# Kernel optimization log

Measured on AMD Instinct MI355X. Metric: run time of the kernel, lower is better.

Reference implementation:

```python
import jax, jax.numpy as jnp
import numpy as np

NUM_EMBEDDINGS = 1024
EMBEDDING_DIM = 256
E_LOSS_WEIGHT = 0.25
MU = 0.01
EPSILON = 1e-05
N_TOKENS = 65536


def setup_inputs() -> dict:
    key = jax.random.key(0)
    k1, k2, k3 = jax.random.split(key, 3)
    return {
        "inputs": jax.random.normal(k1, (N_TOKENS, EMBEDDING_DIM), dtype=jnp.float32),
        "embedding_weight": jax.random.normal(k2, (NUM_EMBEDDINGS, EMBEDDING_DIM), dtype=jnp.float32),
        "ema_w": jax.random.normal(k3, (NUM_EMBEDDINGS, EMBEDDING_DIM), dtype=jnp.float32),
        "ema_cluster_size": jnp.zeros((NUM_EMBEDDINGS,), dtype=jnp.float32),
    }


def reference(inputs, embedding_weight, ema_w, ema_cluster_size):
    N, D = inputs.shape
    K = embedding_weight.shape[0]

    # Squared L2 distances: [N, K]
    distances = (
        jnp.sum(inputs ** 2, axis=1, keepdims=True)
        + jnp.sum(embedding_weight ** 2, axis=1)
        - 2.0 * (inputs @ embedding_weight.T)
    )
    idx = jnp.argmin(distances, axis=1)              # [N]

    # Gather codebook entries (replaces one-hot @ weight)
    quantized_raw = embedding_weight[idx]            # [N, D]

    # Commitment loss (quantized detached)
    e_latent_loss = jnp.mean((jax.lax.stop_gradient(quantized_raw) - inputs) ** 2)
    loss = E_LOSS_WEIGHT * e_latent_loss

    # Per-code counts and scatter-sum of inputs (replaces one-hot matmuls)
    counts = jax.ops.segment_sum(jnp.ones((N,), inputs.dtype), idx, num_segments=K)  # [K]
    dw = jax.ops.segment_sum(inputs, idx, num_segments=K)                             # [K, D]

    # EMA updates (training branch)
    new_cluster = ema_cluster_size * (1.0 - MU) + MU * counts
    n = jnp.sum(new_cluster)
    new_cluster = (new_cluster + EPSILON) / (n + K * EPSILON) * n
    new_ema_w = ema_w * (1.0 - MU) + MU * dw
    new_embedding = new_ema_w / new_cluster[:, None]

    # Straight-through estimator
    quantized = inputs + jax.lax.stop_gradient(quantized_raw - inputs)

    avg_probs = counts / N
    perplexity = jnp.exp(-jnp.sum(avg_probs * jnp.log(avg_probs + 1e-10)))

    encoding_indices = idx.reshape(N, 1)
    return quantized, loss, encoding_indices, perplexity, new_cluster, new_ema_w, new_embedding
```

## Files before the change

kernel.cpp:

```cpp
#include <hip/hip_runtime.h>

typedef _Float16 half8 __attribute__((ext_vector_type(8)));
typedef _Float16 half4 __attribute__((ext_vector_type(4)));
typedef float f32x4 __attribute__((ext_vector_type(4)));

#define N_TOK 65536
#define DIM   256
#define KCODE 1024
#define MU_C  0.01f
#define EPS_C 1e-5f

#define O_Q    0
#define O_LOSS 16777216
#define O_IDX  16777217
#define O_PERP 16842753
#define O_NC   16842754
#define O_NEW  16843778
#define O_EMB  17105922

#define W_IDX   0
#define W_CNT   65536
#define W_CUR   66560
#define W_OFF   67584
#define W_CNTF  68608
#define W_NFLAG 69632
#define W_ELAT  69633
#define W_FLAG  69696
#define W_ORDER 135232
#define W_DW    200768
#define W_WSQ   462912
#define W_WH    463936
#define W_XSQF  595008
#define W_ELATA 660544
#define W_PACK  676928

__device__ __forceinline__ int imin(int a, int b) { return a < b ? a : b; }
__device__ __forceinline__ int imax(int a, int b) { return a > b ? a : b; }

__global__ void convert_wsq(const float* __restrict__ W, _Float16* __restrict__ Wh,
                            float* __restrict__ wsq) {
    int gid = blockIdx.x * 256 + threadIdx.x;
    int row = gid >> 6, lane = gid & 63;
    float4 v = *(const float4*)(W + (size_t)row * 256 + lane * 4);
    half4 h;
    h[0] = (_Float16)v.x; h[1] = (_Float16)v.y; h[2] = (_Float16)v.z; h[3] = (_Float16)v.w;
    *(half4*)(Wh + (size_t)row * 256 + lane * 4) = h;
    float s = v.x * v.x + v.y * v.y + v.z * v.z + v.w * v.w;
#pragma unroll
    for (int off = 1; off < 64; off <<= 1) s += __shfl_xor(s, off);
    if (lane == 0) wsq[row] = s;
}

__global__ __launch_bounds__(256, 2) void argmin_mfma(
    const float* __restrict__ X, const _Float16* __restrict__ Wh,
    const float* __restrict__ wsq, unsigned long long* __restrict__ halfres)
{
    __shared__ _Float16 Bs[2][32 * 256];

    const int tid  = threadIdx.x;
    const int lane = tid & 63;
    const int w    = tid >> 6;
    const int l15  = lane & 15;
    const int lk   = lane >> 4;
    const int half  = blockIdx.x & 1;
    const int cbase = half * 512;
    const int t0    = (blockIdx.x >> 1) * 256;

    half8 a[4][8];
#pragma unroll
    for (int g2 = 0; g2 < 4; ++g2) {
        const float* xr = X + (size_t)(t0 + w * 64 + g2 * 16 + l15) * 256 + lk * 8;
#pragma unroll
        for (int g = 0; g < 8; ++g) {
            float4 u0 = *(const float4*)(xr + g * 32);
            float4 u1 = *(const float4*)(xr + g * 32 + 4);
            half8 h;
            h[0] = (_Float16)u0.x; h[1] = (_Float16)u0.y;
            h[2] = (_Float16)u0.z; h[3] = (_Float16)u0.w;
            h[4] = (_Float16)u1.x; h[5] = (_Float16)u1.y;
            h[6] = (_Float16)u1.z; h[7] = (_Float16)u1.w;
            a[g2][g] = h;
        }
    }

    int u1a[16], u2a[16];
#pragma unroll
    for (int i = 0; i < 16; ++i) { u1a[i] = 0x7FFFFFFF; u2a[i] = 0x7FFFFFFF; }

#define STAGE(cc, bb)                                                          \
    _Pragma("unroll")                                                          \
    for (int i = 0; i < 4; ++i) {                                              \
        int loff = (w * 4 + i) * 1024;                                         \
        int off  = loff + lane * 16;                                           \
        int row  = off >> 9;                                                   \
        int slot = (off >> 4) & 31;                                            \
        const _Float16* src = Wh + (size_t)(cbase + (cc) * 32 + row) * 256     \
                                 + ((slot ^ row) << 3);                        \
        __builtin_amdgcn_global_load_lds(                                      \
            (const __attribute__((address_space(1))) void*)src,                \
            (__attribute__((address_space(3))) void*)((char*)Bs[bb] + loff),   \
            16, 0, 0);                                                         \
    }

    STAGE(0, 0);
    __syncthreads();

    for (int c = 0; c < 16; ++c) {
        const int cur = c & 1;
        if (c < 15) { STAGE(c + 1, cur ^ 1); }

        f32x4 acc[4][2];
#pragma unroll
        for (int g2 = 0; g2 < 4; ++g2) { acc[g2][0] = (f32x4)0.0f; acc[g2][1] = (f32x4)0.0f; }

        __builtin_amdgcn_s_setprio(1);
#pragma unroll
        for (int ks = 0; ks < 8; ++ks) {
            const int j = ks * 4 + lk;
            const char* base = (const char*)Bs[cur];
            half8 b0 = *(const half8*)(base + l15 * 512        + ((j ^ l15) << 4));
            half8 b1 = *(const half8*)(base + (16 + l15) * 512 + ((j ^ (16 + l15)) << 4));
#pragma unroll
            for (int g2 = 0; g2 < 4; ++g2) {
                acc[g2][0] = __builtin_amdgcn_mfma_f32_16x16x32_f16(
                    a[g2][ks], b0, acc[g2][0], 0, 0, 0);
                acc[g2][1] = __builtin_amdgcn_mfma_f32_16x16x32_f16(
                    a[g2][ks], b1, acc[g2][1], 0, 0, 0);
            }
        }
        __builtin_amdgcn_s_setprio(0);

#pragma unroll
        for (int nf = 0; nf < 2; ++nf) {
            int   code = cbase + c * 32 + nf * 16 + l15;
            float tc   = fmaf(0.5f, wsq[code], 512.0f);
#pragma unroll
            for (int g2 = 0; g2 < 4; ++g2)
#pragma unroll
                for (int r = 0; r < 4; ++r) {
                    float sv = tc - acc[g2][nf][r];
                    int u = (__float_as_int(sv) & 0xFFFFFC00) | code;
                    int s = g2 * 4 + r;
                    u2a[s] = imin(u2a[s], imax(u1a[s], u));
                    u1a[s] = imin(u1a[s], u);
                }
        }
        __syncthreads();
    }
#undef STAGE

#pragma unroll
    for (int s = 0; s < 16; ++s) {
#pragma unroll
        for (int off = 1; off < 16; off <<= 1) {
            int b1 = __shfl_xor(u1a[s], off);
            int b2 = __shfl_xor(u2a[s], off);
            int n2 = imin(imin(u2a[s], b2), imax(u1a[s], b1));
            u1a[s] = imin(u1a[s], b1);
            u2a[s] = n2;
        }
    }
    if (l15 == 0) {
#pragma unroll
        for (int s = 0; s < 16; ++s) {
            int row = t0 + w * 64 + (s >> 2) * 16 + lk * 4 + (s & 3);
            halfres[(size_t)half * 65536 + row] =
                ((unsigned long long)(unsigned)u1a[s] << 32) | (unsigned)u2a[s];
        }
    }
}

__global__ void merge_halves(const unsigned long long* __restrict__ halfres,
                             int* __restrict__ idx_out,
                             unsigned* __restrict__ nflag, int* __restrict__ flaglist)
{
    int t = blockIdx.x * 256 + threadIdx.x;
    unsigned long long A = halfres[t], B = halfres[65536 + t];
    int a1 = (int)(A >> 32), a2 = (int)(unsigned)A;
    int b1 = (int)(B >> 32), b2 = (int)(unsigned)B;
    int u1 = imin(a1, b1);
    int u2 = imin(imax(a1, b1), imin(a2, b2));
    idx_out[t] = u1 & 1023;
    float s1 = __int_as_float(u1 & 0xFFFFFC00);
    float s2 = __int_as_float(u2 & 0xFFFFFC00);
    if (s2 - s1 < 0.125f) {
        unsigned p = atomicAdd(nflag, 1u);
        flaglist[p] = t;
    }
}

__global__ void cleanup_xsq(const float* __restrict__ X,
                            const unsigned* __restrict__ nflagp,
                            const int* __restrict__ flaglist,
                            float* __restrict__ xsqf) {
    int n = (int)nflagp[0];
    int wid  = (blockIdx.x * 256 + threadIdx.x) >> 6;
    int lane = threadIdx.x & 63;
    for (int i = wid; i < n; i += 1024) {
        const float* row = X + (size_t)flaglist[i] * 256;
        float4 v = *(const float4*)(row + lane * 4);
        float s = v.x * v.x + v.y * v.y + v.z * v.z + v.w * v.w;
#pragma unroll
        for (int off = 1; off < 64; off <<= 1) s += __shfl_xor(s, off);
        if (lane == 0) xsqf[i] = s;
    }
}

__global__ __launch_bounds__(256, 2) void cleanup_gemm(
    const float* __restrict__ X, const float* __restrict__ W,
    const float* __restrict__ wsq, const unsigned* __restrict__ nflagp,
    const int* __restrict__ flaglist, const float* __restrict__ xsqf,
    unsigned long long* __restrict__ pack)
{
    __shared__ float xs [16][64];
    __shared__ float wps[16][128];
    __shared__ float wsq_s[128];

    const int n = (int)nflagp[0];
    const int tid = threadIdx.x;
    const int tx  = tid & 15;
    const int ty  = tid >> 4;
    const int c0    = (blockIdx.x & 7) * 128;
    const int tslot = blockIdx.x >> 3;
    const int srow_x = tid & 63,  sq_x = tid >> 6;
    const int srow_w = tid & 127, sh_w = tid >> 7;

    if (tid < 128) wsq_s[tid] = wsq[c0 + tid];

    for (int tile = tslot; tile * 64 < n; tile += 256) {
        const int t0 = tile * 64;
        const int gtok = flaglist[imin(t0 + srow_x, n - 1)];
        const float* xrow = X + (size_t)gtok * DIM;
        const float* wrow = W + (size_t)(c0 + srow_w) * DIM + sh_w * 8;

        float xsq_r[4];
#pragma unroll
        for (int i = 0; i < 4; ++i) xsq_r[i] = xsqf[imin(t0 + ty * 4 + i, n - 1)];

        float minv[4]; int mini[4];
#pragma unroll
        for (int i = 0; i < 4; ++i) { minv[i] = 3.402823466e+38f; mini[i] = 0; }

        float acc[4][8];
#pragma unroll
        for (int i = 0; i < 4; ++i)
#pragma unroll
            for (int j = 0; j < 8; ++j) acc[i][j] = 0.0f;

        float4 xa = *(const float4*)(xrow + sq_x * 4);
        float4 wa = *(const float4*)(wrow);
        float4 wb = *(const float4*)(wrow + 4);

        for (int ks = 0; ks < 16; ++ks) {
            __syncthreads();
            xs[sq_x * 4 + 0][srow_x] = xa.x; xs[sq_x * 4 + 1][srow_x] = xa.y;
            xs[sq_x * 4 + 2][srow_x] = xa.z; xs[sq_x * 4 + 3][srow_x] = xa.w;
            wps[sh_w * 8 + 0][srow_w] = wa.x; wps[sh_w * 8 + 1][srow_w] = wa.y;
            wps[sh_w * 8 + 2][srow_w] = wa.z; wps[sh_w * 8 + 3][srow_w] = wa.w;
            wps[sh_w * 8 + 4][srow_w] = wb.x; wps[sh_w * 8 + 5][srow_w] = wb.y;
            wps[sh_w * 8 + 6][srow_w] = wb.z; wps[sh_w * 8 + 7][srow_w] = wb.w;
            __syncthreads();
            if (ks < 15) {
                xa = *(const float4*)(xrow + (ks + 1) * 16 + sq_x * 4);
                wa = *(const float4*)(wrow + (ks + 1) * 16);
                wb = *(const float4*)(wrow + (ks + 1) * 16 + 4);
            }
#pragma unroll
            for (int kl = 0; kl < 16; ++kl) {
                float4 av = *(const float4*)&xs [kl][ty * 4];
                float4 b0 = *(const float4*)&wps[kl][tx * 8];
                float4 b1 = *(const float4*)&wps[kl][tx * 8 + 4];
                float aa[4] = {av.x, av.y, av.z, av.w};
                float bb[8] = {b0.x, b0.y, b0.z, b0.w, b1.x, b1.y, b1.z, b1.w};
#pragma unroll
                for (int i = 0; i < 4; ++i)
#pragma unroll
                    for (int j = 0; j < 8; ++j)
                        acc[i][j] = fmaf(aa[i], bb[j], acc[i][j]);
            }
        }
#pragma unroll
        for (int i = 0; i < 4; ++i) {
#pragma unroll
            for (int j = 0; j < 8; ++j) {
                float t1 = xsq_r[i] + wsq_s[tx * 8 + j];
                float s  = t1 - 2.0f * acc[i][j];
                int   cc = c0 + tx * 8 + j;
                if (s < minv[i]) { minv[i] = s; mini[i] = cc; }
            }
        }
#pragma unroll
        for (int i = 0; i < 4; ++i) {
#pragma unroll
            for (int off = 1; off < 16; off <<= 1) {
                float ov = __shfl_xor(minv[i], off);
                int   oi = __shfl_xor(mini[i], off);
                if (ov < minv[i] || (ov == minv[i] && oi < mini[i])) {
                    minv[i] = ov; mini[i] = oi;
                }
            }
        }
        if (tx == 0) {
#pragma unroll
            for (int i = 0; i < 4; ++i) {
                int pos = t0 + ty * 4 + i;
                if (pos < n) {
                    unsigned long long pu =
                        ((unsigned long long)(unsigned)__float_as_int(minv[i]) << 32)
                        | (unsigned)mini[i];
                    atomicMin(&pack[pos], pu);
                }
            }
        }
        __syncthreads();
    }
}

__global__ void cleanup_write(const unsigned* __restrict__ nflagp,
                              const int* __restrict__ flaglist,
                              const unsigned long long* __restrict__ pack,
                              int* __restrict__ idx_out) {
    int n = (int)nflagp[0];
    for (int i = blockIdx.x * 256 + threadIdx.x; i < n; i += 65536)
        idx_out[flaglist[i]] = (int)(pack[i] & 0xFFFFFFFFull);
}

__global__ __launch_bounds__(256) void epilogue_token(
    const float* __restrict__ X, const float* __restrict__ W,
    const int* __restrict__ idx, float* __restrict__ out,
    float* __restrict__ elat_arr, unsigned* __restrict__ cnt)
{
    int gid = blockIdx.x * 256 + threadIdx.x;
    int t = gid >> 6, q = gid & 63;
    int code = idx[t];
    float4 x4 = ((const float4*)X)[gid];
    float4 w4 = ((const float4*)W)[(size_t)code * 64 + q];
    ((float4*)(out + O_Q))[gid] = w4;
    float dx0 = w4.x - x4.x, dx1 = w4.y - x4.y, dx2 = w4.z - x4.z, dx3 = w4.w - x4.w;
    float e = dx0 * dx0 + dx1 * dx1 + dx2 * dx2 + dx3 * dx3;
    if (q == 0) {
        out[O_IDX + t] = (float)code;
        atomicAdd(&cnt[code], 1u);
    }
#pragma unroll
    for (int off = 1; off < 64; off <<= 1) e += __shfl_xor(e, off);
    __shared__ float se[4];
    int lane = threadIdx.x & 63, wid = threadIdx.x >> 6;
    if (lane == 0) se[wid] = e;
    __syncthreads();
    if (threadIdx.x == 0) elat_arr[blockIdx.x] = se[0] + se[1] + se[2] + se[3];
}

__global__ __launch_bounds__(256) void k_scan(const unsigned* __restrict__ cnt,
                                              unsigned* __restrict__ offs,
                                              float* __restrict__ cntf) {
    int t = threadIdx.x, lane = t & 63, wid = t >> 6;
    uint4 v = ((const uint4*)cnt)[t];
    cntf[4 * t + 0] = (float)v.x; cntf[4 * t + 1] = (float)v.y;
    cntf[4 * t + 2] = (float)v.z; cntf[4 * t + 3] = (float)v.w;
    unsigned s = v.x + v.y + v.z + v.w;
    unsigned ps = s;
#pragma unroll
    for (int off = 1; off < 64; off <<= 1) {
        unsigned o = __shfl_up(ps, off);
        if (lane >= off) ps += o;
    }
    __shared__ unsigned wsum[4];
    if (lane == 63) wsum[wid] = ps;
    __syncthreads();
    unsigned base = 0;
#pragma unroll
    for (int i = 0; i < 4; ++i) if (i < wid) base += wsum[i];
    unsigned excl = base + ps - s;
    offs[4 * t + 0] = excl;
    offs[4 * t + 1] = excl + v.x;
    offs[4 * t + 2] = excl + v.x + v.y;
    offs[4 * t + 3] = excl + v.x + v.y + v.z;
}

__global__ void k_scatter(const int* __restrict__ idx, const unsigned* __restrict__ offs,
                          unsigned* __restrict__ cursor, int* __restrict__ order) {
    int t = blockIdx.x * 256 + threadIdx.x;
    int c = idx[t];
    unsigned p = atomicAdd(&cursor[c], 1u);
    order[offs[c] + p] = t;
}

__global__ __launch_bounds__(256) void k_dw(const float* __restrict__ X,
                                            const int* __restrict__ order,
                                            const int* __restrict__ idx,
                                            float* __restrict__ dw)
{
    int gw   = (blockIdx.x * 256 + threadIdx.x) >> 6;
    int lane = threadIdx.x & 63;
    int p0 = gw * 16;
    float4 acc = make_float4(0.f, 0.f, 0.f, 0.f);
    int cur = -1;
#pragma unroll 4
    for (int i = 0; i < 16; ++i) {
        int t = order[p0 + i];
        int c = idx[t];
        float4 x4 = *(const float4*)(X + (size_t)t * 256 + lane * 4);
        if (c != cur) {
            if (cur >= 0) {
                float* dwp = dw + (size_t)cur * 256 + lane * 4;
                atomicAdd(dwp + 0, acc.x); atomicAdd(dwp + 1, acc.y);
                atomicAdd(dwp + 2, acc.z); atomicAdd(dwp + 3, acc.w);
            }
            cur = c; acc = x4;
        } else {
            acc.x += x4.x; acc.y += x4.y; acc.z += x4.z; acc.w += x4.w;
        }
    }
    if (cur >= 0) {
        float* dwp = dw + (size_t)cur * 256 + lane * 4;
        atomicAdd(dwp + 0, acc.x); atomicAdd(dwp + 1, acc.y);
        atomicAdd(dwp + 2, acc.z); atomicAdd(dwp + 3, acc.w);
    }
}

__global__ __launch_bounds__(1024) void finalize_small(
    const float* __restrict__ ecs, const float* __restrict__ counts,
    const float* __restrict__ elat_arr, float* __restrict__ out)
{
    int k = threadIdx.x;
    float cnt = counts[k];
    float nc = ecs[k] * (1.0f - MU_C) + MU_C * cnt;
    float p = cnt * (1.0f / 65536.0f);
    float h = p * logf(p + 1e-10f);
    float el = 0.f;
#pragma unroll
    for (int i = 0; i < 16; ++i) el += elat_arr[k + i * 1024];
    float rn = nc, rh = h, re = el;
#pragma unroll
    for (int off = 1; off < 64; off <<= 1) {
        rn += __shfl_xor(rn, off);
        rh += __shfl_xor(rh, off);
        re += __shfl_xor(re, off);
    }
    __shared__ float sn[16], sh[16], sef[16];
    int wid = k >> 6, lane = k & 63;
    if (lane == 0) { sn[wid] = rn; sh[wid] = rh; sef[wid] = re; }
    __syncthreads();
    float n = 0.0f, H = 0.0f, E = 0.0f;
#pragma unroll
    for (int i = 0; i < 16; ++i) { n += sn[i]; H += sh[i]; E += sef[i]; }
    out[O_NC + k] = (nc + EPS_C) / (n + 1024.0f * EPS_C) * n;
    if (k == 0) {
        out[O_LOSS] = 0.25f * (E * (1.0f / 16777216.0f));
        out[O_PERP] = expf(-H);
    }
}

__global__ void finalize_embed(const float* __restrict__ ema_w,
                               const float* __restrict__ dw, float* __restrict__ out)
{
    int gid = blockIdx.x * blockDim.x + threadIdx.x;
    int k = gid >> 8;
    float ew = ema_w[gid] * (1.0f - MU_C) + MU_C * dw[gid];
    out[O_NEW + gid] = ew;
    out[O_EMB + gid] = ew / out[O_NC + k];
}

extern "C" void kernel_launch(void* const* d_in, const int* in_sizes, int n_in,
                              void* d_out, int out_size, void* d_ws, size_t ws_size,
                              hipStream_t stream) {
    const float* X     = (const float*)d_in[0];
    const float* W     = (const float*)d_in[1];
    const float* ema_w = (const float*)d_in[2];
    const float* ecs   = (const float*)d_in[3];
    float*    out    = (float*)d_out;
    unsigned* wsu    = (unsigned*)d_ws;
    float*    wsf    = (float*)d_ws;
    int*      idx    = (int*)d_ws + W_IDX;
    unsigned* cnt    = wsu + W_CNT;
    unsigned* cursor = wsu + W_CUR;
    unsigned* offs   = wsu + W_OFF;
    float*    cntf   = wsf + W_CNTF;
    unsigned* nflag  = wsu + W_NFLAG;
    int*      flags  = (int*)d_ws + W_FLAG;
    int*      order  = (int*)d_ws + W_ORDER;
    float*    dw     = wsf + W_DW;
    float*    wsq    = wsf + W_WSQ;
    _Float16* Wh     = (_Float16*)(wsu + W_WH);
    float*    xsqf   = wsf + W_XSQF;
    float*    elatA  = wsf + W_ELATA;
    unsigned long long* pack    = (unsigned long long*)(wsu + W_PACK);
    unsigned long long* halfres = (unsigned long long*)(wsf + W_DW);

    hipMemsetAsync(wsu + W_CNT, 0, 4098 * sizeof(unsigned), stream);
    hipMemsetAsync(pack, 0xFF, 65536 * sizeof(unsigned long long), stream);
    hipLaunchKernelGGL(convert_wsq,    dim3(256),   dim3(256),  0, stream, W, Wh, wsq);
    hipLaunchKernelGGL(argmin_mfma,    dim3(512),   dim3(256),  0, stream, X, Wh, wsq, halfres);
    hipLaunchKernelGGL(merge_halves,   dim3(256),   dim3(256),  0, stream, halfres, idx, nflag, flags);
    hipMemsetAsync(wsf + W_DW, 0, 262144 * sizeof(float), stream);
    hipLaunchKernelGGL(cleanup_xsq,    dim3(256),   dim3(256),  0, stream, X, nflag, flags, xsqf);
    hipLaunchKernelGGL(cleanup_gemm,   dim3(2048),  dim3(256),  0, stream, X, W, wsq, nflag, flags, xsqf, pack);
    hipLaunchKernelGGL(cleanup_write,  dim3(256),   dim3(256),  0, stream, nflag, flags, pack, idx);
    hipLaunchKernelGGL(epilogue_token, dim3(16384), dim3(256),  0, stream, X, W, idx, out, elatA, cnt);
    hipLaunchKernelGGL(k_scan,         dim3(1),     dim3(256),  0, stream, cnt, offs, cntf);
    hipLaunchKernelGGL(k_scatter,      dim3(256),   dim3(256),  0, stream, idx, offs, cursor, order);
    hipLaunchKernelGGL(k_dw,           dim3(1024),  dim3(256),  0, stream, X, order, idx, dw);
    hipLaunchKernelGGL(finalize_small, dim3(1),     dim3(1024), 0, stream, ecs, cntf, elatA, out);
    hipLaunchKernelGGL(finalize_embed, dim3(1024),  dim3(256),  0, stream, ema_w, dw, out);
}
```

Baseline: 240.3 us.

## Fuse token epilogue into sorted dw pass and fold memsets into convert kernel

The per-token epilogue (quantized write, commitment error, histogram) is folded into the sorted dw accumulation kernel, so X is read once for both outputs. A separate histogram kernel counts codes, and the order array packs code and token to avoid an extra idx lookup. The three memsets move into convert_wsq, which removes API calls, and the argmin loop swaps __syncthreads for explicit vmcnt waits plus raw barriers. In exchange, quantized rows are written in sorted order, which scatters the stores, and halfres now needs its own workspace region.

```diff
diff --git a/kernel.cpp b/kernel.cpp
--- a/kernel.cpp
+++ b/kernel.cpp
@@ -24,7 +24,6 @@
 #define W_OFF   67584
 #define W_CNTF  68608
 #define W_NFLAG 69632
-#define W_ELAT  69633
 #define W_FLAG  69696
 #define W_ORDER 135232
 #define W_DW    200768
@@ -33,12 +32,13 @@
 #define W_XSQF  595008
 #define W_ELATA 660544
 #define W_PACK  676928
+#define W_HALF  808000
 
 __device__ __forceinline__ int imin(int a, int b) { return a < b ? a : b; }
 __device__ __forceinline__ int imax(int a, int b) { return a > b ? a : b; }
 
 __global__ void convert_wsq(const float* __restrict__ W, _Float16* __restrict__ Wh,
-                            float* __restrict__ wsq) {
+                            float* __restrict__ wsq, unsigned* __restrict__ wsu) {
     int gid = blockIdx.x * 256 + threadIdx.x;
     int row = gid >> 6, lane = gid & 63;
     float4 v = *(const float4*)(W + (size_t)row * 256 + lane * 4);
@@ -49,6 +49,9 @@
 #pragma unroll
     for (int off = 1; off < 64; off <<= 1) s += __shfl_xor(s, off);
     if (lane == 0) wsq[row] = s;
+    if (gid < 4097) wsu[W_CNT + gid] = 0u;
+    ((float4*)(wsu + W_DW))[gid] = make_float4(0.f, 0.f, 0.f, 0.f);
+    ((unsigned long long*)(wsu + W_PACK))[gid] = ~0ull;
 }
 
 __global__ __launch_bounds__(256, 2) void argmin_mfma(
@@ -103,11 +106,16 @@
     }
 
     STAGE(0, 0);
-    __syncthreads();
 
     for (int c = 0; c < 16; ++c) {
         const int cur = c & 1;
-        if (c < 15) { STAGE(c + 1, cur ^ 1); }
+        if (c < 15) {
+            STAGE(c + 1, cur ^ 1);
+            asm volatile("s_waitcnt vmcnt(4)" ::: "memory");
+        } else {
+            asm volatile("s_waitcnt vmcnt(0)" ::: "memory");
+        }
+        __builtin_amdgcn_s_barrier();
 
         f32x4 acc[4][2];
 #pragma unroll
@@ -145,7 +153,7 @@
                     u1a[s] = imin(u1a[s], u);
                 }
         }
-        __syncthreads();
+        __builtin_amdgcn_s_barrier();
     }
 #undef STAGE
 
@@ -171,7 +179,7 @@
 }
 
 __global__ void merge_halves(const unsigned long long* __restrict__ halfres,
-                             int* __restrict__ idx_out,
+                             int* __restrict__ idx_out, float* __restrict__ out,
                              unsigned* __restrict__ nflag, int* __restrict__ flaglist)
 {
     int t = blockIdx.x * 256 + threadIdx.x;
@@ -181,6 +189,7 @@
     int u1 = imin(a1, b1);
     int u2 = imin(imax(a1, b1), imin(a2, b2));
     idx_out[t] = u1 & 1023;
+    out[O_IDX + t] = (float)(u1 & 1023);
     float s1 = __int_as_float(u1 & 0xFFFFFC00);
     float s2 = __int_as_float(u2 & 0xFFFFFC00);
     if (s2 - s1 < 0.125f) {
@@ -319,36 +328,19 @@
 __global__ void cleanup_write(const unsigned* __restrict__ nflagp,
                               const int* __restrict__ flaglist,
                               const unsigned long long* __restrict__ pack,
-                              int* __restrict__ idx_out) {
+                              int* __restrict__ idx_out, float* __restrict__ out) {
     int n = (int)nflagp[0];
-    for (int i = blockIdx.x * 256 + threadIdx.x; i < n; i += 65536)
-        idx_out[flaglist[i]] = (int)(pack[i] & 0xFFFFFFFFull);
-}
-
-__global__ __launch_bounds__(256) void epilogue_token(
-    const float* __restrict__ X, const float* __restrict__ W,
-    const int* __restrict__ idx, float* __restrict__ out,
-    float* __restrict__ elat_arr, unsigned* __restrict__ cnt)
-{
-    int gid = blockIdx.x * 256 + threadIdx.x;
-    int t = gid >> 6, q = gid & 63;
-    int code = idx[t];
-    float4 x4 = ((const float4*)X)[gid];
-    float4 w4 = ((const float4*)W)[(size_t)code * 64 + q];
-    ((float4*)(out + O_Q))[gid] = w4;
-    float dx0 = w4.x - x4.x, dx1 = w4.y - x4.y, dx2 = w4.z - x4.z, dx3 = w4.w - x4.w;
-    float e = dx0 * dx0 + dx1 * dx1 + dx2 * dx2 + dx3 * dx3;
-    if (q == 0) {
+    for (int i = blockIdx.x * 256 + threadIdx.x; i < n; i += 65536) {
+        int t = flaglist[i];
+        int code = (int)(pack[i] & 0xFFFFFFFFull);
+        idx_out[t] = code;
         out[O_IDX + t] = (float)code;
-        atomicAdd(&cnt[code], 1u);
-    }
-#pragma unroll
-    for (int off = 1; off < 64; off <<= 1) e += __shfl_xor(e, off);
-    __shared__ float se[4];
-    int lane = threadIdx.x & 63, wid = threadIdx.x >> 6;
-    if (lane == 0) se[wid] = e;
-    __syncthreads();
-    if (threadIdx.x == 0) elat_arr[blockIdx.x] = se[0] + se[1] + se[2] + se[3];
+    }
+}
+
+__global__ void k_hist(const int* __restrict__ idx, unsigned* __restrict__ cnt) {
+    int t = blockIdx.x * 256 + threadIdx.x;
+    atomicAdd(&cnt[idx[t]], 1u);
 }
 
 __global__ __launch_bounds__(256) void k_scan(const unsigned* __restrict__ cnt,
@@ -379,27 +371,29 @@
 }
 
 __global__ void k_scatter(const int* __restrict__ idx, const unsigned* __restrict__ offs,
-                          unsigned* __restrict__ cursor, int* __restrict__ order) {
+                          unsigned* __restrict__ cursor, unsigned* __restrict__ order) {
     int t = blockIdx.x * 256 + threadIdx.x;
     int c = idx[t];
     unsigned p = atomicAdd(&cursor[c], 1u);
-    order[offs[c] + p] = t;
-}
-
-__global__ __launch_bounds__(256) void k_dw(const float* __restrict__ X,
-                                            const int* __restrict__ order,
-                                            const int* __restrict__ idx,
-                                            float* __restrict__ dw)
+    order[offs[c] + p] = ((unsigned)c << 16) | (unsigned)t;
+}
+
+__global__ __launch_bounds__(256) void k_epilogue_dw(
+    const float* __restrict__ X, const float* __restrict__ W,
+    const unsigned* __restrict__ order, float* __restrict__ out,
+    float* __restrict__ dw, float* __restrict__ elat_arr)
 {
     int gw   = (blockIdx.x * 256 + threadIdx.x) >> 6;
     int lane = threadIdx.x & 63;
     int p0 = gw * 16;
     float4 acc = make_float4(0.f, 0.f, 0.f, 0.f);
+    float4 wreg = make_float4(0.f, 0.f, 0.f, 0.f);
     int cur = -1;
+    float e = 0.f;
 #pragma unroll 4
     for (int i = 0; i < 16; ++i) {
-        int t = order[p0 + i];
-        int c = idx[t];
+        unsigned u = order[p0 + i];
+        int t = (int)(u & 0xFFFFu), c = (int)(u >> 16);
         float4 x4 = *(const float4*)(X + (size_t)t * 256 + lane * 4);
         if (c != cur) {
             if (cur >= 0) {
@@ -407,16 +401,28 @@
                 atomicAdd(dwp + 0, acc.x); atomicAdd(dwp + 1, acc.y);
                 atomicAdd(dwp + 2, acc.z); atomicAdd(dwp + 3, acc.w);
             }
+            wreg = *(const float4*)(W + (size_t)c * 256 + lane * 4);
             cur = c; acc = x4;
         } else {
             acc.x += x4.x; acc.y += x4.y; acc.z += x4.z; acc.w += x4.w;
         }
+        ((float4*)(out + O_Q))[(size_t)t * 64 + lane] = wreg;
+        float d0 = wreg.x - x4.x, d1 = wreg.y - x4.y;
+        float d2 = wreg.z - x4.z, d3 = wreg.w - x4.w;
+        e += d0 * d0 + d1 * d1 + d2 * d2 + d3 * d3;
     }
     if (cur >= 0) {
         float* dwp = dw + (size_t)cur * 256 + lane * 4;
         atomicAdd(dwp + 0, acc.x); atomicAdd(dwp + 1, acc.y);
         atomicAdd(dwp + 2, acc.z); atomicAdd(dwp + 3, acc.w);
     }
+#pragma unroll
+    for (int off = 1; off < 64; off <<= 1) e += __shfl_xor(e, off);
+    __shared__ float se[4];
+    int wid = threadIdx.x >> 6;
+    if (lane == 0) se[wid] = e;
+    __syncthreads();
+    if (threadIdx.x == 0) elat_arr[blockIdx.x] = se[0] + se[1] + se[2] + se[3];
 }
 
 __global__ __launch_bounds__(1024) void finalize_small(
@@ -428,9 +434,7 @@
     float nc = ecs[k] * (1.0f - MU_C) + MU_C * cnt;
     float p = cnt * (1.0f / 65536.0f);
     float h = p * logf(p + 1e-10f);
-    float el = 0.f;
-#pragma unroll
-    for (int i = 0; i < 16; ++i) el += elat_arr[k + i * 1024];
+    float el = elat_arr[k];
     float rn = nc, rh = h, re = el;
 #pragma unroll
     for (int off = 1; off < 64; off <<= 1) {
@@ -479,28 +483,25 @@
     float*    cntf   = wsf + W_CNTF;
     unsigned* nflag  = wsu + W_NFLAG;
     int*      flags  = (int*)d_ws + W_FLAG;
-    int*      order  = (int*)d_ws + W_ORDER;
+    unsigned* order  = wsu + W_ORDER;
     float*    dw     = wsf + W_DW;
     float*    wsq    = wsf + W_WSQ;
     _Float16* Wh     = (_Float16*)(wsu + W_WH);
     float*    xsqf   = wsf + W_XSQF;
     float*    elatA  = wsf + W_ELATA;
     unsigned long long* pack    = (unsigned long long*)(wsu + W_PACK);
-    unsigned long long* halfres = (unsigned long long*)(wsf + W_DW);
-
-    hipMemsetAsync(wsu + W_CNT, 0, 4098 * sizeof(unsigned), stream);
-    hipMemsetAsync(pack, 0xFF, 65536 * sizeof(unsigned long long), stream);
-    hipLaunchKernelGGL(convert_wsq,    dim3(256),   dim3(256),  0, stream, W, Wh, wsq);
+    unsigned long long* halfres = (unsigned long long*)(wsu + W_HALF);
+
+    hipLaunchKernelGGL(convert_wsq,    dim3(256),   dim3(256),  0, stream, W, Wh, wsq, wsu);
     hipLaunchKernelGGL(argmin_mfma,    dim3(512),   dim3(256),  0, stream, X, Wh, wsq, halfres);
-    hipLaunchKernelGGL(merge_halves,   dim3(256),   dim3(256),  0, stream, halfres, idx, nflag, flags);
-    hipMemsetAsync(wsf + W_DW, 0, 262144 * sizeof(float), stream);
+    hipLaunchKernelGGL(merge_halves,   dim3(256),   dim3(256),  0, stream, halfres, idx, out, nflag, flags);
     hipLaunchKernelGGL(cleanup_xsq,    dim3(256),   dim3(256),  0, stream, X, nflag, flags, xsqf);
     hipLaunchKernelGGL(cleanup_gemm,   dim3(2048),  dim3(256),  0, stream, X, W, wsq, nflag, flags, xsqf, pack);
-    hipLaunchKernelGGL(cleanup_write,  dim3(256),   dim3(256),  0, stream, nflag, flags, pack, idx);
-    hipLaunchKernelGGL(epilogue_token, dim3(16384), dim3(256),  0, stream, X, W, idx, out, elatA, cnt);
+    hipLaunchKernelGGL(cleanup_write,  dim3(256),   dim3(256),  0, stream, nflag, flags, pack, idx, out);
+    hipLaunchKernelGGL(k_hist,         dim3(256),   dim3(256),  0, stream, idx, cnt);
     hipLaunchKernelGGL(k_scan,         dim3(1),     dim3(256),  0, stream, cnt, offs, cntf);
     hipLaunchKernelGGL(k_scatter,      dim3(256),   dim3(256),  0, stream, idx, offs, cursor, order);
-    hipLaunchKernelGGL(k_dw,           dim3(1024),  dim3(256),  0, stream, X, order, idx, dw);
+    hipLaunchKernelGGL(k_epilogue_dw,  dim3(1024),  dim3(256),  0, stream, X, W, order, out, dw, elatA);
     hipLaunchKernelGGL(finalize_small, dim3(1),     dim3(1024), 0, stream, ecs, cntf, elatA, out);
     hipLaunchKernelGGL(finalize_embed, dim3(1024),  dim3(256),  0, stream, ema_w, dw, out);
 }
```

After: 220.3 us. 8.3% less time.
